# Kernel optimization log

Hardware: AMD Instinct MI355X
Metric: run time of the kernel (lower is better)

The kernel has to match this reference:

```python
import jax, jax.numpy as jnp
import numpy as np
from jax.experimental.ode import odeint

OBS_DIM, LATENT_DIM, HIDDEN_DIM = 64, 3, 128
T, B = 200, 4096
NUM_ENCODE = 50
DYN_H = 100


def setup_inputs() -> dict:
    key = jax.random.key(0)
    ks = jax.random.split(key, 20)
    def rn(k, shape, fan_in):
        return (jax.random.normal(k, shape, jnp.float32) / np.float32(np.sqrt(fan_in)))
    return {
        "observations": jax.random.normal(ks[0], (T, B, OBS_DIM), jnp.float32),
        "epsilon": jax.random.normal(ks[1], (B, LATENT_DIM), jnp.float32),
        # GRU params (PyTorch layout: W_ih [3H, in], W_hh [3H, H])
        "gru_Wih": rn(ks[2], (3 * HIDDEN_DIM, OBS_DIM), OBS_DIM),
        "gru_Whh": rn(ks[3], (3 * HIDDEN_DIM, HIDDEN_DIM), HIDDEN_DIM),
        "gru_bih": jnp.zeros((3 * HIDDEN_DIM,), jnp.float32),
        "gru_bhh": jnp.zeros((3 * HIDDEN_DIM,), jnp.float32),
        "mean_W": rn(ks[4], (LATENT_DIM, HIDDEN_DIM), HIDDEN_DIM),
        "mean_b": jnp.zeros((LATENT_DIM,), jnp.float32),
        "logvar_W": rn(ks[5], (LATENT_DIM, HIDDEN_DIM), HIDDEN_DIM),
        "logvar_b": jnp.zeros((LATENT_DIM,), jnp.float32),
        # dynamics MLP 3->100->100->3
        "dyn_W1": rn(ks[6], (DYN_H, LATENT_DIM), LATENT_DIM),
        "dyn_b1": jnp.zeros((DYN_H,), jnp.float32),
        "dyn_W2": rn(ks[7], (DYN_H, DYN_H), DYN_H),
        "dyn_b2": jnp.zeros((DYN_H,), jnp.float32),
        "dyn_W3": rn(ks[8], (LATENT_DIM, DYN_H), DYN_H),
        "dyn_b3": jnp.zeros((LATENT_DIM,), jnp.float32),
        # decoder MLP latent->64->obs
        "dec_W1": rn(ks[9], (64, LATENT_DIM), LATENT_DIM),
        "dec_b1": jnp.zeros((64,), jnp.float32),
        "dec_W2": rn(ks[10], (OBS_DIM, 64), 64),
        "dec_b2": jnp.zeros((OBS_DIM,), jnp.float32),
        "time_steps": jnp.arange(T, dtype=jnp.float32) * jnp.float32(0.01),
    }


def _gru_last(x, Wih, Whh, bih, bhh):
    # x: [T, B, obs_dim]; PyTorch GRU cell math, zero initial state
    H = Whh.shape[1]
    def step(h, xt):
        gi = xt @ Wih.T + bih          # [B, 3H]
        gh = h @ Whh.T + bhh           # [B, 3H]
        i_r, i_z, i_n = jnp.split(gi, 3, axis=-1)
        h_r, h_z, h_n = jnp.split(gh, 3, axis=-1)
        r = jax.nn.sigmoid(i_r + h_r)
        z = jax.nn.sigmoid(i_z + h_z)
        n = jnp.tanh(i_n + r * h_n)
        return (1.0 - z) * n + z * h, None
    h0 = jnp.zeros((x.shape[1], H), x.dtype)
    h_last, _ = jax.lax.scan(step, h0, x)
    return h_last


def reference(observations, epsilon, gru_Wih, gru_Whh, gru_bih, gru_bhh,
              mean_W, mean_b, logvar_W, logvar_b,
              dyn_W1, dyn_b1, dyn_W2, dyn_b2, dyn_W3, dyn_b3,
              dec_W1, dec_b1, dec_W2, dec_b2, time_steps):
    h_last = _gru_last(observations[:NUM_ENCODE], gru_Wih, gru_Whh, gru_bih, gru_bhh)
    z0_mean = h_last @ mean_W.T + mean_b
    z0_logvar = h_last @ logvar_W.T + logvar_b
    std = jnp.exp(0.5 * z0_logvar)
    z0 = z0_mean + epsilon * std

    def dyn(z, t):
        h = jnp.tanh(z @ dyn_W1.T + dyn_b1)
        h = jnp.tanh(h @ dyn_W2.T + dyn_b2)
        return h @ dyn_W3.T + dyn_b3

    # dopri5 adaptive solver (torchdiffeq default tolerances)
    traj = odeint(dyn, z0, time_steps, rtol=1e-7, atol=1e-9)  # [T, B, latent]
    h = jax.nn.relu(traj @ dec_W1.T + dec_b1)
    recon = h @ dec_W2.T + dec_b2                              # [T, B, obs]
    return recon, z0_mean, z0_logvar, traj
```

## Files before the change

### kernel.cpp

```cpp
#include <hip/hip_runtime.h>
#include <stddef.h>

#define OFF_MEAN 52428800
#define OFF_LV   52441088
#define OFF_TRAJ 52453376

typedef _Float16 f16x8 __attribute__((ext_vector_type(8)));
typedef _Float16 f16x4 __attribute__((ext_vector_type(4)));
typedef float    f32x4 __attribute__((ext_vector_type(4)));

#define MFMA16(a, b, c) __builtin_amdgcn_mfma_f32_16x16x32_f16((a), (b), (c), 0, 0, 0)

__device__ __forceinline__ float sigm_(float x) {
    float e = __builtin_amdgcn_exp2f(x * -1.442695041f);
    return __builtin_amdgcn_rcpf(1.f + e);
}
__device__ __forceinline__ float tanh_(float x) {
    float e = __builtin_amdgcn_exp2f(x * 2.885390082f);
    return 1.f - 2.f * __builtin_amdgcn_rcpf(e + 1.f);
}
__device__ __forceinline__ float dot4_(float4 a, float4 b) {
    return a.x * b.x + a.y * b.y + a.z * b.z + a.w * b.w;
}

__global__ __launch_bounds__(512, 2) void k_gru(
    const float* __restrict__ obs, const float* __restrict__ eps,
    const float* __restrict__ Wih, const float* __restrict__ Whh,
    const float* __restrict__ bih, const float* __restrict__ bhh,
    const float* __restrict__ meanW, const float* __restrict__ meanB,
    const float* __restrict__ lvW,  const float* __restrict__ lvB,
    float* __restrict__ o_mean, float* __restrict__ o_lv, float* __restrict__ z0)
{
    __shared__ alignas(16) unsigned short h_s[2][2048];
    __shared__ alignas(16) unsigned short x_s[2][1024];
    __shared__ alignas(16) float hm_s[16 * 132];
    __shared__ float mb_s[96];

    const int tid  = threadIdx.x;
    const int b0   = blockIdx.x * 16;
    const int lane = tid & 63, wv = tid >> 6;
    const int lrow = lane & 15, lkb = lane >> 4;
    const int swX  = (lrow & 7) << 4;
    const int swH  = lrow << 4;
    const int u    = wv * 16 + lrow;

    const float bR  = bih[u]       + bhh[u];
    const float bZ  = bih[128 + u] + bhh[128 + u];
    const float bNi = bih[256 + u];
    const float bNh = bhh[256 + u];

    f16x8 wihf[3][2];
    #pragma unroll
    for (int g = 0; g < 3; ++g) {
        int col = g * 128 + u;
        #pragma unroll
        for (int ks = 0; ks < 2; ++ks) {
            const float* wp = Wih + col * 64 + ks * 32 + lkb * 8;
            float4 a = *(const float4*)wp, b = *(const float4*)(wp + 4);
            float tmp[8] = {a.x, a.y, a.z, a.w, b.x, b.y, b.z, b.w};
            f16x8 hv;
            #pragma unroll
            for (int j = 0; j < 8; ++j) hv[j] = (_Float16)tmp[j];
            wihf[g][ks] = hv;
        }
    }
    f16x8 whhh[3][4];
    #pragma unroll
    for (int g = 0; g < 3; ++g) {
        int col = g * 128 + u;
        #pragma unroll
        for (int ks = 0; ks < 4; ++ks) {
            const float* wp = Whh + col * 128 + ks * 32 + lkb * 8;
            float4 a = *(const float4*)wp, b = *(const float4*)(wp + 4);
            float tmp[8] = {a.x, a.y, a.z, a.w, b.x, b.y, b.z, b.w};
            f16x8 hv;
            #pragma unroll
            for (int j = 0; j < 8; ++j) hv[j] = (_Float16)tmp[j];
            whhh[g][ks] = hv;
        }
    }

    for (int i = tid; i < 2048; i += 512) h_s[0][i] = 0;
    const int srow = tid >> 4, skq = (tid & 15) * 4;
    const int sxb  = srow * 128 + ((skq * 2) ^ ((srow & 7) << 4));
    float4 xn;
    if (tid < 256) {
        xn = *(const float4*)(obs + ((size_t)0 * 4096 + b0 + srow) * 64 + skq);
        f16x4 vh = {(_Float16)xn.x, (_Float16)xn.y, (_Float16)xn.z, (_Float16)xn.w};
        *(f16x4*)((char*)x_s[0] + sxb) = vh;
    }
    f32x4 hold = {0.f, 0.f, 0.f, 0.f};
    __syncthreads();

    for (int t = 0; t < 50; ++t) {
        const int cur = t & 1, nxt = cur ^ 1;
        char* x_c = (char*)x_s[cur];
        char* h_c = (char*)h_s[cur];

        if (tid < 256) {
            int tt = (t < 49) ? t + 1 : t;
            xn = *(const float4*)(obs + ((size_t)tt * 4096 + b0 + srow) * 64 + skq);
        }

        f16x8 xh[2], hh[4];
        #pragma unroll
        for (int ks = 0; ks < 2; ++ks) {
            int off = lrow * 128 + ((ks * 64 + lkb * 16) ^ swX);
            xh[ks] = *(const f16x8*)(x_c + off);
        }
        #pragma unroll
        for (int ks = 0; ks < 4; ++ks) {
            int off = lrow * 256 + ((ks * 64 + lkb * 16) ^ swH);
            hh[ks] = *(const f16x8*)(h_c + off);
        }

        f32x4 z4 = {0.f, 0.f, 0.f, 0.f};
        f32x4 aR = z4, aZ = z4, aNi = z4, aNh = z4;
        #pragma unroll
        for (int ks = 0; ks < 2; ++ks) {
            aR  = MFMA16(xh[ks], wihf[0][ks], aR);
            aZ  = MFMA16(xh[ks], wihf[1][ks], aZ);
            aNi = MFMA16(xh[ks], wihf[2][ks], aNi);
        }
        #pragma unroll
        for (int ks = 0; ks < 4; ++ks) {
            aR  = MFMA16(hh[ks], whhh[0][ks], aR);
            aZ  = MFMA16(hh[ks], whhh[1][ks], aZ);
            aNh = MFMA16(hh[ks], whhh[2][ks], aNh);
        }

        char* hn_c = (char*)h_s[nxt];
        #pragma unroll
        for (int i = 0; i < 4; ++i) {
            float r  = sigm_(aR[i] + bR);
            float zg = sigm_(aZ[i] + bZ);
            float n  = tanh_(aNi[i] + bNi + r * (aNh[i] + bNh));
            float hv = (1.f - zg) * n + zg * hold[i];
            hold[i] = hv;
            int ri = lkb * 4 + i;
            int hb = ri * 256 + ((u * 2) ^ (ri << 4));
            *(_Float16*)(hn_c + hb) = (_Float16)hv;
        }

        if (tid < 256 && t < 49) {
            f16x4 vh = {(_Float16)xn.x, (_Float16)xn.y, (_Float16)xn.z, (_Float16)xn.w};
            *(f16x4*)((char*)x_s[nxt] + sxb) = vh;
        }
        __syncthreads();
    }

    #pragma unroll
    for (int i = 0; i < 4; ++i)
        hm_s[(lkb * 4 + i) * 132 + u] = hold[i];
    __syncthreads();

    if (tid < 96) {
        int rr = tid / 6, c = tid - rr * 6, j = (c < 3) ? c : c - 3;
        const float* W = (c < 3) ? meanW : lvW;
        const float* B = (c < 3) ? meanB : lvB;
        float acc = B[j];
        const float4* W4 = (const float4*)(W + j * 128);
        const float4* h4 = (const float4*)(hm_s + rr * 132);
        #pragma unroll 4
        for (int kc = 0; kc < 32; ++kc) acc += dot4_(W4[kc], h4[kc]);
        mb_s[rr * 6 + c] = acc;
    }
    __syncthreads();
    if (tid < 48) {
        int rr = tid / 3, j = tid - rr * 3;
        int gb = b0 + rr;
        float m  = mb_s[rr * 6 + j];
        float lv = mb_s[rr * 6 + j + 3];
        o_mean[gb * 3 + j] = m;
        o_lv[gb * 3 + j]   = lv;
        z0[gb * 3 + j]     = m + eps[gb * 3 + j] * __expf(0.5f * lv);
    }
}

__global__ __launch_bounds__(256, 2) void k_odec(
    const float* __restrict__ dW1, const float* __restrict__ db1,
    const float* __restrict__ dW2, const float* __restrict__ db2,
    const float* __restrict__ dW3, const float* __restrict__ db3,
    const float* __restrict__ decW1, const float* __restrict__ decb1,
    const float* __restrict__ decW2, const float* __restrict__ decb2,
    const float* __restrict__ z0, float* __restrict__ traj, float* __restrict__ recon)
{
    __shared__ alignas(16) unsigned short h1h_s[2048];
    __shared__ alignas(16) unsigned short hd_s[16384];
    __shared__ alignas(16) float h2f[8 * 104];
    __shared__ alignas(16) float W3s[312];
    __shared__ alignas(16) float zbuf[128 * 4];
    __shared__ float w1ds[192], b1ds[64];
    __shared__ float b2s[100], b3s[3];
    __shared__ float fparts[24];

    const int tid  = threadIdx.x;
    const int b0   = blockIdx.x * 8;
    const int lane = tid & 63, wv = tid >> 6;
    const int r    = tid >> 5;
    char* h1h_c = (char*)h1h_s;
    char* hd_c  = (char*)hd_s;

    for (int i = tid; i < 512; i += 256)
        ((unsigned int*)(h1h_c + 2048))[i] = 0u;
    if (tid < 32) h2f[(tid >> 2) * 104 + 100 + (tid & 3)] = 0.f;
    for (int i = tid; i < 312; i += 256) {
        int j = i / 104, k = i - j * 104;
        W3s[i] = (k < 100) ? dW3[j * 100 + k] : 0.f;
    }
    if (tid < 100) b2s[tid] = db2[tid];
    if (tid < 3)   b3s[tid] = db3[tid];
    if (tid < 192) w1ds[tid] = decW1[tid];
    if (tid < 64)  b1ds[tid] = decb1[tid];

    float w1r[12], b1r[4];
    {
        int k0 = (tid & 31) * 4;
        #pragma unroll
        for (int i = 0; i < 4; ++i) {
            int k = k0 + i;
            if (k < 100) {
                w1r[3 * i + 0] = dW1[k * 3 + 0];
                w1r[3 * i + 1] = dW1[k * 3 + 1];
                w1r[3 * i + 2] = dW1[k * 3 + 2];
                b1r[i] = db1[k];
            } else {
                w1r[3 * i + 0] = 0.f; w1r[3 * i + 1] = 0.f; w1r[3 * i + 2] = 0.f;
                b1r[i] = 0.f;
            }
        }
    }
    const int lrow = lane & 15, lkb = lane >> 4;
    const int swA  = (lrow & 7) << 4;

    f16x8 w2h[2][4];
    #pragma unroll
    for (int tile = 0; tile < 2; ++tile) {
        int col = (wv * 2 + tile) * 16 + lrow;
        #pragma unroll
        for (int ks = 0; ks < 4; ++ks) {
            f16x8 hv;
            #pragma unroll
            for (int j = 0; j < 8; ++j) {
                int k = ks * 32 + lkb * 8 + j;
                float v = (col < 100 && k < 100) ? dW2[col * 100 + k] : 0.f;
                hv[j] = (_Float16)v;
            }
            w2h[tile][ks] = hv;
        }
    }
    const int colD = wv * 16 + lrow;
    f16x8 dbh[2];
    #pragma unroll
    for (int ks = 0; ks < 2; ++ks) {
        const float* wp = decW2 + colD * 64 + ks * 32 + lkb * 8;
        float4 a = *(const float4*)wp, b = *(const float4*)(wp + 4);
        float tmp[8] = {a.x, a.y, a.z, a.w, b.x, b.y, b.z, b.w};
        f16x8 hv;
        #pragma unroll
        for (int j = 0; j < 8; ++j) hv[j] = (_Float16)tmp[j];
        dbh[ks] = hv;
    }
    const float dbo = decb2[colD];

    float yv0 = z0[(b0 + r) * 3 + 0];
    float yv1 = z0[(b0 + r) * 3 + 1];
    float yv2 = z0[(b0 + r) * 3 + 2];
    float ka0, ka1, ka2, k10, k11, k12, yn0, yn1, yn2;
    __syncthreads();

#define FEVAL(yt0_, yt1_, yt2_)                                                  \
    do {                                                                          \
        {                                                                         \
            int q = tid & 31, k0 = q * 4;                                         \
            f16x4 hh_;                                                            \
            _Pragma("unroll")                                                     \
            for (int i = 0; i < 4; ++i) {                                         \
                float acc = b1r[i] + w1r[3 * i] * (yt0_)                          \
                          + w1r[3 * i + 1] * (yt1_) + w1r[3 * i + 2] * (yt2_);    \
                hh_[i] = (_Float16)tanh_(acc);                                    \
            }                                                                     \
            int off = r * 256 + ((k0 * 2) ^ (r << 4));                            \
            *(f16x4*)(h1h_c + off) = hh_;                                         \
        }                                                                         \
        __syncthreads();                                                          \
        {                                                                         \
            f16x8 ah[4];                                                          \
            _Pragma("unroll")                                                     \
            for (int ks = 0; ks < 4; ++ks) {                                      \
                int off = lrow * 256 + ((ks * 64 + lkb * 16) ^ swA);              \
                ah[ks] = *(const f16x8*)(h1h_c + off);                            \
            }                                                                     \
            f32x4 acc0 = {0.f, 0.f, 0.f, 0.f}, acc1 = {0.f, 0.f, 0.f, 0.f};       \
            _Pragma("unroll")                                                     \
            for (int ks = 0; ks < 4; ++ks) {                                      \
                acc0 = MFMA16(ah[ks], w2h[0][ks], acc0);                          \
                acc1 = MFMA16(ah[ks], w2h[1][ks], acc1);                          \
            }                                                                     \
            if (lkb < 2) {                                                        \
                int r0 = lkb * 4;                                                 \
                _Pragma("unroll")                                                 \
                for (int tile = 0; tile < 2; ++tile) {                            \
                    int col = (wv * 2 + tile) * 16 + lrow;                        \
                    f32x4 a = tile ? acc1 : acc0;                                 \
                    if (col < 100) {                                              \
                        float bb = b2s[col];                                      \
                        _Pragma("unroll")                                         \
                        for (int i = 0; i < 4; ++i)                               \
                            h2f[(r0 + i) * 104 + col] = tanh_(a[i] + bb);         \
                    }                                                             \
                }                                                                 \
            }                                                                     \
        }                                                                         \
        __syncthreads();                                                          \
        {                                                                         \
            if (tid < 96) {                                                       \
                int rr = tid / 12, rem = tid - rr * 12, j = rem >> 2, qc = rem & 3;\
                const float4* Wj = (const float4*)(W3s + j * 104);                \
                const float4* Hr = (const float4*)(h2f + rr * 104);               \
                float acc = 0.f;                                                  \
                _Pragma("unroll")                                                 \
                for (int kc = 0; kc < 7; ++kc) {                                  \
                    int k = qc + kc * 4;                                          \
                    if (k < 26) acc += dot4_(Wj[k], Hr[k]);                       \
                }                                                                 \
                acc += __shfl_xor(acc, 1);                                        \
                acc += __shfl_xor(acc, 2);                                        \
                if (qc == 0) fparts[rr * 3 + j] = acc + b3s[j];                   \
            }                                                                     \
        }                                                                         \
        __syncthreads();                                                          \
    } while (0)

    FEVAL(yv0, yv1, yv2);

    #pragma unroll 1
    for (int s = 0; s < 13; ++s) {
        const int   npts = (s < 12) ? 16 : 8;
        const float hh   = (s < 12) ? 0.16f : 0.07f;
        const int   t0   = s * 16;
        const float invN = (s < 12) ? 0.0625f : (1.f / 7.f);

        float f0_ = fparts[r * 3 + 0], f1_ = fparts[r * 3 + 1], f2_ = fparts[r * 3 + 2];
        k10 = f0_; k11 = f1_; k12 = f2_;
        ka0 = f0_; ka1 = f1_; ka2 = f2_;
        float yt0 = yv0 + 0.5f * hh * f0_, yt1 = yv1 + 0.5f * hh * f1_, yt2 = yv2 + 0.5f * hh * f2_;
        FEVAL(yt0, yt1, yt2);
        f0_ = fparts[r * 3 + 0]; f1_ = fparts[r * 3 + 1]; f2_ = fparts[r * 3 + 2];
        ka0 += 2.f * f0_; ka1 += 2.f * f1_; ka2 += 2.f * f2_;
        yt0 = yv0 + 0.5f * hh * f0_; yt1 = yv1 + 0.5f * hh * f1_; yt2 = yv2 + 0.5f * hh * f2_;
        FEVAL(yt0, yt1, yt2);
        f0_ = fparts[r * 3 + 0]; f1_ = fparts[r * 3 + 1]; f2_ = fparts[r * 3 + 2];
        ka0 += 2.f * f0_; ka1 += 2.f * f1_; ka2 += 2.f * f2_;
        yt0 = yv0 + hh * f0_; yt1 = yv1 + hh * f1_; yt2 = yv2 + hh * f2_;
        FEVAL(yt0, yt1, yt2);
        f0_ = fparts[r * 3 + 0]; f1_ = fparts[r * 3 + 1]; f2_ = fparts[r * 3 + 2];
        ka0 += f0_; ka1 += f1_; ka2 += f2_;
        const float h6 = hh * (1.f / 6.f);
        yn0 = yv0 + h6 * ka0; yn1 = yv1 + h6 * ka1; yn2 = yv2 + h6 * ka2;
        FEVAL(yn0, yn1, yn2);
        float fn0 = fparts[r * 3 + 0], fn1 = fparts[r * 3 + 1], fn2 = fparts[r * 3 + 2];

        {
            int tot = 3 * npts;
            for (int ii = (tid & 31); ii < tot; ii += 32) {
                int q = ii / 3, j = ii - q * 3;
                float ysj = (j == 0) ? yv0 : (j == 1) ? yv1 : yv2;
                float f0j = (j == 0) ? k10 : (j == 1) ? k11 : k12;
                float ynj = (j == 0) ? yn0 : (j == 1) ? yn1 : yn2;
                float fnj = (j == 0) ? fn0 : (j == 1) ? fn1 : fn2;
                float th  = (float)q * invN;
                float th2 = th * th, th3 = th2 * th;
                float ca = 2.f * th3 - 3.f * th2 + 1.f;
                float cb = th3 - 2.f * th2 + th;
                float cc = 3.f * th2 - 2.f * th3;
                float cd = th3 - th2;
                float v = ca * ysj + cb * hh * f0j + cc * ynj + cd * hh * fnj;
                traj[((size_t)(t0 + q) * 4096 + b0 + r) * 3 + j] = v;
                zbuf[(q * 8 + r) * 4 + j] = v;
            }
        }
        __syncthreads();

        {
            const int p  = tid >> 1;
            const int u0 = (tid & 1) * 32;
            if (p < npts * 8) {
                const float z0v = zbuf[p * 4 + 0], z1v = zbuf[p * 4 + 1], z2v = zbuf[p * 4 + 2];
                const int sw = (p & 7) << 4;
                #pragma unroll
                for (int c = 0; c < 8; ++c) {
                    f16x4 hh_;
                    #pragma unroll
                    for (int i = 0; i < 4; ++i) {
                        int u = u0 + c * 4 + i;
                        float acc = b1ds[u] + w1ds[u * 3 + 0] * z0v
                                            + w1ds[u * 3 + 1] * z1v
                                            + w1ds[u * 3 + 2] * z2v;
                        hh_[i] = (_Float16)fmaxf(acc, 0.f);
                    }
                    int off = p * 128 + (((u0 + c * 4) * 2) ^ sw);
                    *(f16x4*)(hd_c + off) = hh_;
                }
            }
        }
        __syncthreads();

        {
            const int nrt = (npts * 8) >> 4;
            for (int rt = 0; rt < nrt; ++rt) {
                f16x8 a0, a1;
                {
                    int base = (rt * 16 + lrow) * 128;
                    a0 = *(const f16x8*)(hd_c + base + ((0 + lkb * 16) ^ swA));
                    a1 = *(const f16x8*)(hd_c + base + ((64 + lkb * 16) ^ swA));
                }
                f32x4 acc = {0.f, 0.f, 0.f, 0.f};
                acc = MFMA16(a0, dbh[0], acc);
                acc = MFMA16(a1, dbh[1], acc);
                #pragma unroll
                for (int i = 0; i < 4; ++i) {
                    int pr = rt * 16 + lkb * 4 + i;
                    int q = pr >> 3, row = pr & 7;
                    recon[((size_t)(t0 + q) * 4096 + b0 + row) * 64 + colD] = acc[i] + dbo;
                }
            }
        }
        yv0 = yn0; yv1 = yn1; yv2 = yn2;
    }
#undef FEVAL
}

extern "C" void kernel_launch(void* const* d_in, const int* in_sizes, int n_in,
                              void* d_out, int out_size, void* d_ws, size_t ws_size,
                              hipStream_t stream)
{
    const float* obs   = (const float*)d_in[0];
    const float* eps   = (const float*)d_in[1];
    const float* Wih   = (const float*)d_in[2];
    const float* Whh   = (const float*)d_in[3];
    const float* bih   = (const float*)d_in[4];
    const float* bhh   = (const float*)d_in[5];
    const float* meanW = (const float*)d_in[6];
    const float* meanB = (const float*)d_in[7];
    const float* lvW   = (const float*)d_in[8];
    const float* lvB   = (const float*)d_in[9];
    const float* dW1   = (const float*)d_in[10];
    const float* db1   = (const float*)d_in[11];
    const float* dW2   = (const float*)d_in[12];
    const float* db2   = (const float*)d_in[13];
    const float* dW3   = (const float*)d_in[14];
    const float* db3   = (const float*)d_in[15];
    const float* decW1 = (const float*)d_in[16];
    const float* decb1 = (const float*)d_in[17];
    const float* decW2 = (const float*)d_in[18];
    const float* decb2 = (const float*)d_in[19];

    float* out   = (float*)d_out;
    float* recon = out;
    float* omean = out + OFF_MEAN;
    float* olv   = out + OFF_LV;
    float* traj  = out + OFF_TRAJ;
    float* z0    = (float*)d_ws;

    k_gru<<<dim3(256), dim3(512), 0, stream>>>(obs, eps, Wih, Whh, bih, bhh,
                                               meanW, meanB, lvW, lvB, omean, olv, z0);
    k_odec<<<dim3(512), dim3(256), 0, stream>>>(dW1, db1, dW2, db2, dW3, db3,
                                                decW1, decb1, decW2, decb2,
                                                z0, traj, recon);
}
```

Before: 164.7 us.

## Fuse dynamics output layer into MFMA epilogue with shuffle reduction

The third dynamics layer (100->3) is now computed directly from the MFMA accumulators. Each lane applies tanh, multiplies by W3 weights kept in registers, and reduces across 16 lanes with xor shuffles. Each wave writes partial sums to a small double-buffered LDS array, and each row sums the four wave partials. This removes the h2 LDS round trip, the separate reduction stage and one __syncthreads per function evaluation, and it also shrinks LDS usage. The cost is 48 extra shuffles per evaluation and more registers per thread.

```diff
diff --git a/kernel.cpp b/kernel.cpp
--- a/kernel.cpp
+++ b/kernel.cpp
@@ -185,40 +185,32 @@
     const float* __restrict__ decW2, const float* __restrict__ decb2,
     const float* __restrict__ z0, float* __restrict__ traj, float* __restrict__ recon)
 {
-    __shared__ alignas(16) unsigned short h1h_s[2048];
-    __shared__ alignas(16) unsigned short hd_s[16384];
-    __shared__ alignas(16) float h2f[8 * 104];
-    __shared__ alignas(16) float W3s[312];
+    __shared__ alignas(16) unsigned short h1_s[2048];
+    __shared__ alignas(16) unsigned short hd_s[8192];
     __shared__ alignas(16) float zbuf[128 * 4];
+    __shared__ alignas(16) float fp2[2][96];
     __shared__ float w1ds[192], b1ds[64];
-    __shared__ float b2s[100], b3s[3];
-    __shared__ float fparts[24];
 
     const int tid  = threadIdx.x;
     const int b0   = blockIdx.x * 8;
     const int lane = tid & 63, wv = tid >> 6;
     const int r    = tid >> 5;
-    char* h1h_c = (char*)h1h_s;
-    char* hd_c  = (char*)hd_s;
+    const int lrow = lane & 15, lkb = lane >> 4;
+    const int swA  = (lrow & 7) << 4;
+    char* h1c = (char*)h1_s;
+    char* hdc = (char*)hd_s;
 
     for (int i = tid; i < 512; i += 256)
-        ((unsigned int*)(h1h_c + 2048))[i] = 0u;
-    if (tid < 32) h2f[(tid >> 2) * 104 + 100 + (tid & 3)] = 0.f;
-    for (int i = tid; i < 312; i += 256) {
-        int j = i / 104, k = i - j * 104;
-        W3s[i] = (k < 100) ? dW3[j * 100 + k] : 0.f;
-    }
-    if (tid < 100) b2s[tid] = db2[tid];
-    if (tid < 3)   b3s[tid] = db3[tid];
+        ((unsigned int*)(h1c + 2048))[i] = 0u;
     if (tid < 192) w1ds[tid] = decW1[tid];
     if (tid < 64)  b1ds[tid] = decb1[tid];
 
     float w1r[12], b1r[4];
     {
-        int k0 = (tid & 31) * 4;
+        int k0q = (tid & 31) * 4;
         #pragma unroll
         for (int i = 0; i < 4; ++i) {
-            int k = k0 + i;
+            int k = k0q + i;
             if (k < 100) {
                 w1r[3 * i + 0] = dW1[k * 3 + 0];
                 w1r[3 * i + 1] = dW1[k * 3 + 1];
@@ -230,9 +222,6 @@
             }
         }
     }
-    const int lrow = lane & 15, lkb = lane >> 4;
-    const int swA  = (lrow & 7) << 4;
-
     f16x8 w2h[2][4];
     #pragma unroll
     for (int tile = 0; tile < 2; ++tile) {
@@ -249,6 +238,18 @@
             w2h[tile][ks] = hv;
         }
     }
+    float w3r[6], b2r[2], b3r[3];
+    #pragma unroll
+    for (int tile = 0; tile < 2; ++tile) {
+        int col = (wv * 2 + tile) * 16 + lrow;
+        b2r[tile] = (col < 100) ? db2[col] : 0.f;
+        #pragma unroll
+        for (int j = 0; j < 3; ++j)
+            w3r[tile * 3 + j] = (col < 100) ? dW3[j * 100 + col] : 0.f;
+    }
+    #pragma unroll
+    for (int j = 0; j < 3; ++j) b3r[j] = db3[j];
+
     const int colD = wv * 16 + lrow;
     f16x8 dbh[2];
     #pragma unroll
@@ -266,70 +267,72 @@
     float yv0 = z0[(b0 + r) * 3 + 0];
     float yv1 = z0[(b0 + r) * 3 + 1];
     float yv2 = z0[(b0 + r) * 3 + 2];
-    float ka0, ka1, ka2, k10, k11, k12, yn0, yn1, yn2;
+    float fc0, fc1, fc2;
+    float k10, k11, k12, ka0, ka1, ka2, yn0, yn1, yn2;
+    int pb = 0;
     __syncthreads();
 
-#define FEVAL(yt0_, yt1_, yt2_)                                                  \
+#define FEVAL(yt0_, yt1_, yt2_)                                                   \
     do {                                                                          \
-        {                                                                         \
-            int q = tid & 31, k0 = q * 4;                                         \
-            f16x4 hh_;                                                            \
+        {                 \
+            int k0q = (tid & 31) * 4;                                             \
+            f16x4 hh_;                                                           \
             _Pragma("unroll")                                                     \
             for (int i = 0; i < 4; ++i) {                                         \
-                float acc = b1r[i] + w1r[3 * i] * (yt0_)                          \
-                          + w1r[3 * i + 1] * (yt1_) + w1r[3 * i + 2] * (yt2_);    \
-                hh_[i] = (_Float16)tanh_(acc);                                    \
+                float a_ = b1r[i] + w1r[3 * i] * (yt0_)                           \
+                         + w1r[3 * i + 1] * (yt1_) + w1r[3 * i + 2] * (yt2_);     \
+                hh_[i] = (_Float16)tanh_(a_);                                     \
             }                                                                     \
-            int off = r * 256 + ((k0 * 2) ^ (r << 4));                            \
-            *(f16x4*)(h1h_c + off) = hh_;                                         \
+            *(f16x4*)(h1c + r * 256 + ((k0q * 2) ^ (r << 4))) = hh_;              \
         }                                                                         \
         __syncthreads();                                                          \
-        {                                                                         \
+        {           \
             f16x8 ah[4];                                                          \
             _Pragma("unroll")                                                     \
-            for (int ks = 0; ks < 4; ++ks) {                                      \
-                int off = lrow * 256 + ((ks * 64 + lkb * 16) ^ swA);              \
-                ah[ks] = *(const f16x8*)(h1h_c + off);                            \
-            }                                                                     \
+            for (int ks = 0; ks < 4; ++ks)                                        \
+                ah[ks] = *(const f16x8*)(h1c + lrow * 256 + ((ks * 64 + lkb * 16) ^ swA)); \
             f32x4 acc0 = {0.f, 0.f, 0.f, 0.f}, acc1 = {0.f, 0.f, 0.f, 0.f};       \
             _Pragma("unroll")                                                     \
             for (int ks = 0; ks < 4; ++ks) {                                      \
                 acc0 = MFMA16(ah[ks], w2h[0][ks], acc0);                          \
                 acc1 = MFMA16(ah[ks], w2h[1][ks], acc1);                          \
             }                                                                     \
-            if (lkb < 2) {                                                        \
-                int r0 = lkb * 4;                                                 \
+            float part[12];                                                       \
+            _Pragma("unroll")                                                     \
+            for (int v = 0; v < 12; ++v) part[v] = 0.f;                           \
+            _Pragma("unroll")                                                     \
+            for (int i = 0; i < 4; ++i) {                                         \
+                float h2a = tanh_(acc0[i] + b2r[0]);                              \
+                float h2b = tanh_(acc1[i] + b2r[1]);                              \
                 _Pragma("unroll")                                                 \
-                for (int tile = 0; tile < 2; ++tile) {                            \
-                    int col = (wv * 2 + tile) * 16 + lrow;                        \
-                    f32x4 a = tile ? acc1 : acc0;                                 \
-                    if (col < 100) {                                              \
-                        float bb = b2s[col];                                      \
-                        _Pragma("unroll")                                         \
-                        for (int i = 0; i < 4; ++i)                               \
-                            h2f[(r0 + i) * 104 + col] = tanh_(a[i] + bb);         \
-                    }                                                             \
+                for (int j = 0; j < 3; ++j)                                       \
+                    part[j * 4 + i] += w3r[j] * h2a + w3r[3 + j] * h2b;           \
+            }                                                                     \
+            _Pragma("unroll")                                                     \
+            for (int mk = 1; mk <= 8; mk <<= 1) {                                 \
+                _Pragma("unroll")                                                 \
+                for (int v = 0; v < 12; ++v)                                      \
+                    part[v] += __shfl_xor(part[v], mk);                           \
+            }                                                                     \
+            if (lrow == 0 && lkb < 2) {                                           \
+                _Pragma("unroll")                                                 \
+                for (int i = 0; i < 4; ++i) {                                     \
+                    _Pragma("unroll")                                             \
+                    for (int j = 0; j < 3; ++j)                                   \
+                        fp2[pb][((lkb * 4 + i) * 3 + j) * 4 + wv] = part[j * 4 + i]; \
                 }                                                                 \
             }                                                                     \
         }                                                                         \
         __syncthreads();                                                          \
-        {                                                                         \
-            if (tid < 96) {                                                       \
-                int rr = tid / 12, rem = tid - rr * 12, j = rem >> 2, qc = rem & 3;\
-                const float4* Wj = (const float4*)(W3s + j * 104);                \
-                const float4* Hr = (const float4*)(h2f + rr * 104);               \
-                float acc = 0.f;                                                  \
-                _Pragma("unroll")                                                 \
-                for (int kc = 0; kc < 7; ++kc) {                                  \
-                    int k = qc + kc * 4;                                          \
-                    if (k < 26) acc += dot4_(Wj[k], Hr[k]);                       \
-                }                                                                 \
-                acc += __shfl_xor(acc, 1);                                        \
-                acc += __shfl_xor(acc, 2);                                        \
-                if (qc == 0) fparts[rr * 3 + j] = acc + b3s[j];                   \
-            }                                                                     \
+        {                                    \
+            f32x4 s0 = *(const f32x4*)&fp2[pb][(r * 3 + 0) * 4];                  \
+            f32x4 s1 = *(const f32x4*)&fp2[pb][(r * 3 + 1) * 4];                  \
+            f32x4 s2 = *(const f32x4*)&fp2[pb][(r * 3 + 2) * 4];                  \
+            fc0 = s0[0] + s0[1] + s0[2] + s0[3] + b3r[0];                         \
+            fc1 = s1[0] + s1[1] + s1[2] + s1[3] + b3r[1];                         \
+            fc2 = s2[0] + s2[1] + s2[2] + s2[3] + b3r[2];                         \
         }                                                                         \
-        __syncthreads();                                                          \
+        pb ^= 1;                                                                  \
     } while (0)
 
     FEVAL(yv0, yv1, yv2);
@@ -341,25 +344,20 @@
         const int   t0   = s * 16;
         const float invN = (s < 12) ? 0.0625f : (1.f / 7.f);
 
-        float f0_ = fparts[r * 3 + 0], f1_ = fparts[r * 3 + 1], f2_ = fparts[r * 3 + 2];
-        k10 = f0_; k11 = f1_; k12 = f2_;
-        ka0 = f0_; ka1 = f1_; ka2 = f2_;
-        float yt0 = yv0 + 0.5f * hh * f0_, yt1 = yv1 + 0.5f * hh * f1_, yt2 = yv2 + 0.5f * hh * f2_;
+        k10 = fc0; k11 = fc1; k12 = fc2;
+        ka0 = fc0; ka1 = fc1; ka2 = fc2;
+        float yt0 = yv0 + 0.5f * hh * fc0, yt1 = yv1 + 0.5f * hh * fc1, yt2 = yv2 + 0.5f * hh * fc2;
         FEVAL(yt0, yt1, yt2);
-        f0_ = fparts[r * 3 + 0]; f1_ = fparts[r * 3 + 1]; f2_ = fparts[r * 3 + 2];
-        ka0 += 2.f * f0_; ka1 += 2.f * f1_; ka2 += 2.f * f2_;
-        yt0 = yv0 + 0.5f * hh * f0_; yt1 = yv1 + 0.5f * hh * f1_; yt2 = yv2 + 0.5f * hh * f2_;
+        ka0 += 2.f * fc0; ka1 += 2.f * fc1; ka2 += 2.f * fc2;
+        yt0 = yv0 + 0.5f * hh * fc0; yt1 = yv1 + 0.5f * hh * fc1; yt2 = yv2 + 0.5f * hh * fc2;
         FEVAL(yt0, yt1, yt2);
-        f0_ = fparts[r * 3 + 0]; f1_ = fparts[r * 3 + 1]; f2_ = fparts[r * 3 + 2];
-        ka0 += 2.f * f0_; ka1 += 2.f * f1_; ka2 += 2.f * f2_;
-        yt0 = yv0 + hh * f0_; yt1 = yv1 + hh * f1_; yt2 = yv2 + hh * f2_;
+        ka0 += 2.f * fc0; ka1 += 2.f * fc1; ka2 += 2.f * fc2;
+        yt0 = yv0 + hh * fc0; yt1 = yv1 + hh * fc1; yt2 = yv2 + hh * fc2;
         FEVAL(yt0, yt1, yt2);
-        f0_ = fparts[r * 3 + 0]; f1_ = fparts[r * 3 + 1]; f2_ = fparts[r * 3 + 2];
-        ka0 += f0_; ka1 += f1_; ka2 += f2_;
+        ka0 += fc0; ka1 += fc1; ka2 += fc2;
         const float h6 = hh * (1.f / 6.f);
         yn0 = yv0 + h6 * ka0; yn1 = yv1 + h6 * ka1; yn2 = yv2 + h6 * ka2;
         FEVAL(yn0, yn1, yn2);
-        float fn0 = fparts[r * 3 + 0], fn1 = fparts[r * 3 + 1], fn2 = fparts[r * 3 + 2];
 
         {
             int tot = 3 * npts;
@@ -368,7 +366,7 @@
                 float ysj = (j == 0) ? yv0 : (j == 1) ? yv1 : yv2;
                 float f0j = (j == 0) ? k10 : (j == 1) ? k11 : k12;
                 float ynj = (j == 0) ? yn0 : (j == 1) ? yn1 : yn2;
-                float fnj = (j == 0) ? fn0 : (j == 1) ? fn1 : fn2;
+                float fnj = (j == 0) ? fc0 : (j == 1) ? fc1 : fc2;
                 float th  = (float)q * invN;
                 float th2 = th * th, th3 = th2 * th;
                 float ca = 2.f * th3 - 3.f * th2 + 1.f;
@@ -400,7 +398,7 @@
                         hh_[i] = (_Float16)fmaxf(acc, 0.f);
                     }
                     int off = p * 128 + (((u0 + c * 4) * 2) ^ sw);
-                    *(f16x4*)(hd_c + off) = hh_;
+                    *(f16x4*)(hdc + off) = hh_;
                 }
             }
         }
@@ -412,8 +410,8 @@
                 f16x8 a0, a1;
                 {
                     int base = (rt * 16 + lrow) * 128;
-                    a0 = *(const f16x8*)(hd_c + base + ((0 + lkb * 16) ^ swA));
-                    a1 = *(const f16x8*)(hd_c + base + ((64 + lkb * 16) ^ swA));
+                    a0 = *(const f16x8*)(hdc + base + ((0 + lkb * 16) ^ swA));
+                    a1 = *(const f16x8*)(hdc + base + ((64 + lkb * 16) ^ swA));
                 }
                 f32x4 acc = {0.f, 0.f, 0.f, 0.f};
                 acc = MFMA16(a0, dbh[0], acc);
```

Result: slower. 189.6 us (+15.1%).
